# Performance work log

Measured on AMD Instinct MI355X. Metric: run time of the kernel, lower is better.

The kernel has to match this reference:

```python
import jax, jax.numpy as jnp
import numpy as np

N_U, N_D = 64, 64
N_E = N_U + N_D
N_A = 32
N_SV, N_PV = 512, 64
# n1 = [4*N_A, N_SV, N_SV, N_SV]; n2 = [4, N_PV, N_PV, N_PV]


def setup_inputs() -> dict:
    key = jax.random.key(0)
    ks = jax.random.split(key, 32)
    n1 = [4 * N_A, N_SV, N_SV, N_SV]
    n2 = [4, N_PV, N_PV, N_PV]
    d = {}
    d['r'] = jax.random.normal(ks[0], (N_E, 3), jnp.float32)
    d['a'] = jax.random.normal(ks[1], (N_A, 3), jnp.float32)
    i = 2
    for l in range(3):
        fin = 3 * n1[l] + 2 * n2[l]
        d[f'V{l}_w'] = jax.random.normal(ks[i], (fin, n1[l + 1]), jnp.float32) / np.float32(np.sqrt(fin)); i += 1
        d[f'V{l}_b'] = jax.random.normal(ks[i], (n1[l + 1],), jnp.float32); i += 1
        d[f'W{l}_w'] = jax.random.normal(ks[i], (n2[l], n2[l + 1]), jnp.float32) / np.float32(np.sqrt(n2[l])); i += 1
        d[f'W{l}_b'] = jax.random.normal(ks[i], (n2[l + 1],), jnp.float32); i += 1
    fin = 3 * N_SV + 2 * N_PV
    d['after_w'] = jax.random.normal(ks[i], (fin, N_SV), jnp.float32) / np.float32(np.sqrt(fin)); i += 1
    d['after_b'] = jax.random.normal(ks[i], (N_SV,), jnp.float32); i += 1
    d['vhu_w'] = jax.random.normal(ks[i], (N_SV, N_SV // 2), jnp.float32) / np.float32(np.sqrt(N_SV)); i += 1
    d['vhu_b'] = jax.random.normal(ks[i], (N_SV // 2,), jnp.float32); i += 1
    d['vhd_w'] = jax.random.normal(ks[i], (N_SV, N_SV // 2), jnp.float32) / np.float32(np.sqrt(N_SV)); i += 1
    d['vhd_b'] = jax.random.normal(ks[i], (N_SV // 2,), jnp.float32); i += 1
    d['wu_w'] = jax.random.normal(ks[i], (N_SV // 2, N_U), jnp.float32) / np.float32(np.sqrt(N_SV // 2)); i += 1
    d['wu_b'] = jax.random.normal(ks[i], (N_U,), jnp.float32); i += 1
    d['wd_w'] = jax.random.normal(ks[i], (N_SV // 2, N_D), jnp.float32) / np.float32(np.sqrt(N_SV // 2)); i += 1
    d['wd_b'] = jax.random.normal(ks[i], (N_D,), jnp.float32); i += 1
    return d


def _fb_block(s_v, p_v):
    # s_v: (N_E, f_s), p_v: (N_E, N_E, f_p)
    s_u_mean = jnp.tile(s_v[:N_U].mean(0)[None, :], (N_E, 1))
    s_d_mean = jnp.tile(s_v[N_U:].mean(0)[None, :], (N_E, 1))
    p_u_mean = p_v[:N_U].mean(0)  # (N_E, f_p)
    p_d_mean = p_v[N_U:].mean(0)
    return jnp.concatenate([s_u_mean, s_d_mean, p_u_mean, p_d_mean, s_v], axis=-1)


def _forward(r, a, Vw, Vb, Ww, Wb, after_w, after_b, vhu_w, vhu_b, vhd_w, vhd_b, wu_w, wu_b, wd_w, wd_b):
    eye = jnp.eye(N_E, dtype=r.dtype)[:, :, None]
    ra = r[:, None, :] - a[None, :, :]                       # (N_E, N_A, 3)
    ra_len = jnp.linalg.norm(ra, axis=-1, keepdims=True)     # (N_E, N_A, 1)
    rr = r[None, :, :] - r[:, None, :]                       # (N_E, N_E, 3)
    rr_len = jnp.linalg.norm(rr + eye, axis=-1, keepdims=True) * (1.0 - eye)
    s_v = jnp.concatenate([ra, ra_len], axis=-1).reshape(N_E, -1)  # (N_E, 4*N_A)
    p_v = jnp.concatenate([rr, rr_len], axis=-1)                   # (N_E, N_E, 4)
    for vw, vb, ww, wb in zip(Vw, Vb, Ww, Wb):
        s_in = _fb_block(s_v, p_v)
        # NOTE: torch residual `s_v if s_v.shape[-1]==n_sv` never fires here:
        # fb_block output width is 3*n1+2*n2 != n_sv, so it adds zeros.
        s_v = jnp.tanh(s_in @ vw + vb)
        p_new = jnp.tanh(p_v @ ww + wb)
        p_v = p_new + (p_v if p_v.shape[-1] == N_PV else 0.0)
    s_in = _fb_block(s_v, p_v)
    s_v = jnp.tanh(s_in @ after_w + after_b)  # (N_E, N_SV); residual again never fires
    s_u = s_v[:N_U] @ vhu_w + vhu_b
    s_d = s_v[N_U:] @ vhd_w + vhd_b
    s_wu = s_u @ wu_w + wu_b   # (N_U, N_U)
    s_wd = s_d @ wd_w + wd_b   # (N_D, N_D)
    exp_u = jnp.linalg.norm(ra[:N_U], axis=-1, keepdims=True)  # (N_U, N_A, 1)
    exp_d = jnp.linalg.norm(ra[N_U:], axis=-1, keepdims=True)
    orb_u = (s_wu * jnp.exp(-exp_u).sum(axis=1))[None]  # (1, N_U, N_U)
    orb_d = (s_wd * jnp.exp(-exp_d).sum(axis=1))[None]
    # logabssumdet for two (1,n,n) matrices with n>1: no 1x1 dets.
    sgn_u, ld_u = jnp.linalg.slogdet(orb_u)
    sgn_d, ld_d = jnp.linalg.slogdet(orb_d)
    sign = sgn_u * sgn_d
    logdet = ld_u + ld_d        # (1,)
    maxlogdet = logdet.max()
    psi = (sign * jnp.exp(logdet - maxlogdet)).sum()
    return jnp.log(jnp.abs(psi)) + maxlogdet  # scalar log|psi|


def reference(r, a, V0_w, V0_b, V1_w, V1_b, V2_w, V2_b, W0_w, W0_b, W1_w, W1_b, W2_w, W2_b,
              after_w, after_b, vhu_w, vhu_b, vhd_w, vhd_b, wu_w, wu_b, wd_w, wd_b):
    Vw, Vb = [V0_w, V1_w, V2_w], [V0_b, V1_b, V2_b]
    Ww, Wb = [W0_w, W1_w, W2_w], [W0_b, W1_b, W2_b]
    return _forward(r, a, Vw, Vb, Ww, Wb, after_w, after_b,
                    vhu_w, vhu_b, vhd_w, vhd_b, wu_w, wu_b, wd_w, wd_b)
```

## Files before the change

### kernel.cpp

```cpp
#include <hip/hip_runtime.h>
#include <math.h>

#define NSV 512

__device__ void pchain_role(int b, const float* __restrict__ r,
                            const float* __restrict__ apos,
                            const float* __restrict__ W0w, const float* __restrict__ W0b,
                            const float* __restrict__ W1w, const float* __restrict__ W1b,
                            const float* __restrict__ W2w, const float* __restrict__ W2b,
                            float* __restrict__ expv,
                            float* __restrict__ pme1, float* __restrict__ pme2,
                            float* __restrict__ pme3, float* sh)
{
    float* rL    = sh;
    float* W0l   = sh + 384;
    float* aposL = sh + 640;
    float* shex  = sh + 736;
    float* p0c   = sh + 768;
    float* PA    = sh + 1024;
    float* Wbuf  = sh + 5376;
    const int j  = b >> 1, sp = b & 1;
    const int t  = threadIdx.x;
    const int i  = t >> 3;
    const int o0 = (t & 7) * 8;

    if (t < 384) rL[t] = r[t];
    else if (t < 480) aposL[t - 384] = apos[t - 384];
    for (int idx = t; idx < 4096; idx += 512) Wbuf[idx] = W1w[idx];
    if (t < 256) W0l[t] = W0w[t];
    __syncthreads();

    const float rjx = rL[j*3+0], rjy = rL[j*3+1], rjz = rL[j*3+2];
    if (t < 64) {
        const int ii = sp*64 + t;
        float dx = rjx - rL[ii*3+0], dy = rjy - rL[ii*3+1], dz = rjz - rL[ii*3+2];
        float len = (ii == j) ? 0.f : sqrtf(dx*dx + dy*dy + dz*dz);
        p0c[t*4+0]=dx; p0c[t*4+1]=dy; p0c[t*4+2]=dz; p0c[t*4+3]=len;
    } else if (sp == 0 && t < 96) {
        const int k = t - 64;
        float dx = rjx - aposL[k*3+0], dy = rjy - aposL[k*3+1], dz = rjz - aposL[k*3+2];
        shex[k] = expf(-sqrtf(dx*dx + dy*dy + dz*dz));
    }
    __syncthreads();

    {
        const float x0=p0c[i*4+0], x1=p0c[i*4+1], x2=p0c[i*4+2], x3=p0c[i*4+3];
        #pragma unroll
        for (int k = 0; k < 8; ++k) {
            const int o = o0 + k;
            float a = W0b[o];
            a = fmaf(x0, W0l[o],     a);
            a = fmaf(x1, W0l[64+o],  a);
            a = fmaf(x2, W0l[128+o], a);
            a = fmaf(x3, W0l[192+o], a);
            PA[i*68+o] = tanhf(a);
        }
    }
    if (sp == 0 && t == 4) {
        float s = 0.f;
        #pragma unroll 8
        for (int k = 0; k < 32; ++k) s += shex[k];
        expv[j] = s;
    }
    __syncthreads();

    if (t < 64) {
        float s = 0.f;
        #pragma unroll 8
        for (int k = 0; k < 64; ++k) s += PA[k*68 + t];
        pme1[j*128 + sp*64 + t] = s * 0.015625f;
    }
    float acc[8], res[8];
    const float* pa = PA + i*68;
    {
        #pragma unroll
        for (int k = 0; k < 8; ++k) acc[k] = W1b[o0+k];
        #pragma unroll 4
        for (int c = 0; c < 64; ++c) {
            const float av = pa[c];
            const float* wr = Wbuf + c*64 + o0;
            float4 wa = *reinterpret_cast<const float4*>(wr);
            float4 wb = *reinterpret_cast<const float4*>(wr+4);
            acc[0]=fmaf(av,wa.x,acc[0]); acc[1]=fmaf(av,wa.y,acc[1]);
            acc[2]=fmaf(av,wa.z,acc[2]); acc[3]=fmaf(av,wa.w,acc[3]);
            acc[4]=fmaf(av,wb.x,acc[4]); acc[5]=fmaf(av,wb.y,acc[5]);
            acc[6]=fmaf(av,wb.z,acc[6]); acc[7]=fmaf(av,wb.w,acc[7]);
        }
        #pragma unroll
        for (int k = 0; k < 8; ++k) res[k] = pa[o0+k];
    }
    __syncthreads();
    #pragma unroll
    for (int k = 0; k < 8; ++k) PA[i*68+o0+k] = tanhf(acc[k]) + res[k];
    __syncthreads();

    if (t < 64) {
        float s = 0.f;
        #pragma unroll 8
        for (int k = 0; k < 64; ++k) s += PA[k*68 + t];
        pme2[j*128 + sp*64 + t] = s * 0.015625f;
    }
    for (int idx = t; idx < 4096; idx += 512) Wbuf[idx] = W2w[idx];
    __syncthreads();

    {
        #pragma unroll
        for (int k = 0; k < 8; ++k) acc[k] = W2b[o0+k];
        #pragma unroll 4
        for (int c = 0; c < 64; ++c) {
            const float av = pa[c];
            const float* wr = Wbuf + c*64 + o0;
            float4 wa = *reinterpret_cast<const float4*>(wr);
            float4 wb = *reinterpret_cast<const float4*>(wr+4);
            acc[0]=fmaf(av,wa.x,acc[0]); acc[1]=fmaf(av,wa.y,acc[1]);
            acc[2]=fmaf(av,wa.z,acc[2]); acc[3]=fmaf(av,wa.w,acc[3]);
            acc[4]=fmaf(av,wb.x,acc[4]); acc[5]=fmaf(av,wb.y,acc[5]);
            acc[6]=fmaf(av,wb.z,acc[6]); acc[7]=fmaf(av,wb.w,acc[7]);
        }
        #pragma unroll
        for (int k = 0; k < 8; ++k) res[k] = pa[o0+k];
    }
    __syncthreads();
    #pragma unroll
    for (int k = 0; k < 8; ++k) PA[i*68+o0+k] = tanhf(acc[k]) + res[k];
    __syncthreads();

    if (t < 64) {
        float s = 0.f;
        #pragma unroll 8
        for (int k = 0; k < 64; ++k) s += PA[k*68 + t];
        pme3[j*128 + sp*64 + t] = s * 0.015625f;
    }
}

__device__ void a0_role(int ab, const float* __restrict__ r,
                        const float* __restrict__ apos,
                        const float* __restrict__ V0w, const float* __restrict__ V0b,
                        float* __restrict__ svA, float* __restrict__ psA, float* sh)
{
    constexpr int KP = 136, KP2 = 68;
    float* As    = sh;
    float* smL   = sh + 544;
    float* red   = sh + 800;
    float* t1L   = sh + 1312;
    float* rL    = sh + 1376;
    float* aposL = sh + 1760;
    const int t  = threadIdx.x;
    const int et = ab >> 3, e0 = et * 4;
    const int o0 = (ab & 7) * 64;
    const int ol = t & 63, o = o0 + ol;
    const int wv = t >> 6;

    if (t < 384) rL[t] = r[t];
    else if (t < 480) aposL[t - 384] = apos[t - 384];
    __syncthreads();

    if (t < 128) {
        const int e_l = t >> 5, k = t & 31;
        const int e = e0 + e_l;
        float dx = rL[e*3+0]-aposL[k*3+0], dy = rL[e*3+1]-aposL[k*3+1],
              dz = rL[e*3+2]-aposL[k*3+2];
        float len = sqrtf(dx*dx + dy*dy + dz*dz);
        float* dst = As + e_l*KP + 8 + k*4;
        dst[0]=dx; dst[1]=dy; dst[2]=dz; dst[3]=len;
    } else if (t < 160) {
        const int q = t - 128;
        const int e_l = q >> 3, outp = q & 7;
        const int spin = outp >> 2, c = outp & 3;
        const int e = e0 + e_l;
        const float ex = rL[e*3+0], ey = rL[e*3+1], ez = rL[e*3+2];
        float s = 0.f;
        for (int i2 = 0; i2 < 64; ++i2) {
            const int ii = spin*64 + i2;
            float dx = ex - rL[ii*3+0], dy = ey - rL[ii*3+1], dz = ez - rL[ii*3+2];
            float v = (c==0)?dx:(c==1)?dy:(c==2)?dz:
                      ((ii==e)?0.f:sqrtf(dx*dx+dy*dy+dz*dz));
            s += v;
        }
        As[e_l*KP + outp] = s * 0.015625f;
    }
    {
        const int outp = t >> 1, half = t & 1;
        const int spin = outp >> 7, cc = outp & 127, a_i = cc >> 2, d = cc & 3;
        const float ax = aposL[a_i*3+0], ay = aposL[a_i*3+1], az = aposL[a_i*3+2];
        float s = 0.f;
        #pragma unroll 8
        for (int q = 0; q < 32; ++q) {
            const int e = spin*64 + half*32 + q;
            float dx = rL[e*3+0]-ax, dy = rL[e*3+1]-ay, dz = rL[e*3+2]-az;
            float len = sqrtf(dx*dx + dy*dy + dz*dz);
            s += (d==0)?dx:(d==1)?dy:(d==2)?dz:len;
        }
        red[t] = s;
    }
    __syncthreads();
    if (t < 256) smL[t] = (red[2*t] + red[2*t+1]) * 0.015625f;
    __syncthreads();

    {
        float a1 = 0.f;
        const float* Wp = V0w + (size_t)(wv*32)*NSV + o;
        const float* mp = smL + wv*32;
        #pragma unroll 8
        for (int k = 0; k < 32; ++k) a1 = fmaf(mp[k], Wp[(size_t)k*NSV], a1);
        red[wv*64 + ol] = a1;
    }
    __syncthreads();
    if (t < 64) {
        float s = V0b[o0 + t];
        #pragma unroll
        for (int g = 0; g < 8; ++g) s += red[g*64 + t];
        t1L[t] = s;
    }
    __syncthreads();

    const int e_l = wv & 3, kh = wv >> 2;
    {
        float a2 = (kh == 0) ? t1L[ol] : 0.f;
        const float* Ap = As + e_l*KP + kh*KP2;
        const float* Wp = V0w + (size_t)(256 + kh*KP2)*NSV + o;
        #pragma unroll 16
        for (int k = 0; k < KP2; ++k)
            a2 = fmaf(Ap[k], Wp[(size_t)k*NSV], a2);
        red[wv*64 + ol] = a2;
    }
    __syncthreads();
    float v = 0.f;
    if (t < 256) {
        v = tanhf(red[(t>>6)*64 + (t&63)] + red[((t>>6)+4)*64 + (t&63)]);
        svA[(size_t)(e0 + (t>>6))*NSV + o0 + (t&63)] = v;
    }
    __syncthreads();
    if (t < 256) red[t] = v;
    __syncthreads();
    if (t < 64) {
        float s = red[t] + red[64+t] + red[128+t] + red[192+t];
        psA[(size_t)et*NSV + o0 + t] = s;
    }
}

__global__ __launch_bounds__(512)
void front_kernel(const float* __restrict__ r, const float* __restrict__ apos,
                  const float* __restrict__ V0w, const float* __restrict__ V0b,
                  const float* __restrict__ W0w, const float* __restrict__ W0b,
                  const float* __restrict__ W1w, const float* __restrict__ W1b,
                  const float* __restrict__ W2w, const float* __restrict__ W2b,
                  float* __restrict__ svA, float* __restrict__ expv,
                  float* __restrict__ pme1, float* __restrict__ pme2,
                  float* __restrict__ pme3, float* __restrict__ psA)
{
    __shared__ __align__(16) float sh[9472];
    const int b = blockIdx.x;
    if (b < 256)
        pchain_role(b, r, apos, W0w, W0b, W1w, W1b, W2w, W2b,
                    expv, pme1, pme2, pme3, sh);
    else
        a0_role(b - 256, r, apos, V0w, V0b, svA, psA, sh);
}

template<int FS, int FP>
__global__ __launch_bounds__(512)
void a2_kernel(const float* __restrict__ svIn, const float* __restrict__ pmeIn,
               const float* __restrict__ psumIn,
               const float* __restrict__ Vw, const float* __restrict__ Vb,
               float* __restrict__ svOut, float* __restrict__ psumOut)
{
    constexpr int KP  = 2*FP + FS;
    constexpr int KP2 = KP/2;
    __shared__ __align__(16) float As[4*KP];
    __shared__ __align__(16) float smL[2*FS];
    __shared__ __align__(16) float red[512];
    __shared__ float t1L[64];
    const int t  = threadIdx.x;
    const int et = blockIdx.x >> 3;
    const int e0 = et * 4;
    const int o0 = (blockIdx.x & 7) * 64;
    const int ol = t & 63;
    const int o  = o0 + ol;
    const int wv = t >> 6;

    for (int idx = t; idx < 4*2*FP; idx += 512)
        As[(idx/(2*FP))*KP + idx%(2*FP)] =
            pmeIn[(size_t)(e0 + idx/(2*FP))*(2*FP) + idx%(2*FP)];
    for (int idx = t; idx < FS; idx += 512) {
        const int row = idx / (FS/4), c4 = idx % (FS/4);
        *reinterpret_cast<float4*>(&As[row*KP + 2*FP + c4*4]) =
            *reinterpret_cast<const float4*>(&svIn[(size_t)(e0+row)*FS + c4*4]);
    }
    for (int idx = t; idx < 2*FS; idx += 512) {
        const int col = (idx < FS) ? idx : idx - FS;
        const int r0  = (idx < FS) ? 0 : 16;
        const float* base = psumIn + (size_t)r0*NSV + col;
        float s = 0.f;
        #pragma unroll
        for (int k = 0; k < 16; ++k) s += base[(size_t)k*NSV];
        smL[idx] = s * 0.015625f;
    }
    __syncthreads();

    {
        constexpr int TI = (2*FS)/8;
        float a1 = 0.f;
        const float* Wp = Vw + (size_t)(wv*TI)*NSV + o;
        const float* mp = smL + wv*TI;
        #pragma unroll 8
        for (int k = 0; k < TI; ++k) a1 = fmaf(mp[k], Wp[(size_t)k*NSV], a1);
        red[wv*64 + ol] = a1;
    }
    __syncthreads();
    if (t < 64) {
        float s = Vb[o0 + t];
        #pragma unroll
        for (int g = 0; g < 8; ++g) s += red[g*64 + t];
        t1L[t] = s;
    }
    __syncthreads();

    const int e_l = wv & 3, kh = wv >> 2;
    {
        float a2 = (kh == 0) ? t1L[ol] : 0.f;
        const float* Ap = As + e_l*KP + kh*KP2;
        const float* Wp = Vw + (size_t)(2*FS + kh*KP2)*NSV + o;
        #pragma unroll 16
        for (int k = 0; k < KP2; ++k)
            a2 = fmaf(Ap[k], Wp[(size_t)k*NSV], a2);
        red[wv*64 + ol] = a2;
    }
    __syncthreads();
    float v = 0.f;
    if (t < 256) {
        v = tanhf(red[(t>>6)*64 + (t&63)] + red[((t>>6)+4)*64 + (t&63)]);
        svOut[(size_t)(e0 + (t>>6))*NSV + o0 + (t&63)] = v;
    }
    if (psumOut) {
        __syncthreads();
        if (t < 256) red[t] = v;
        __syncthreads();
        if (t < 64) {
            float s = red[t] + red[64+t] + red[128+t] + red[192+t];
            psumOut[(size_t)et*NSV + o0 + t] = s;
        }
    }
}

__global__ __launch_bounds__(512)
void headsw_kernel(const float* __restrict__ svF,
                   const float* __restrict__ vhu_w, const float* __restrict__ vhu_b,
                   const float* __restrict__ vhd_w, const float* __restrict__ vhd_b,
                   const float* __restrict__ wu_w,  const float* __restrict__ wu_b,
                   const float* __restrict__ wd_w,  const float* __restrict__ wd_b,
                   const float* __restrict__ expv,  float* __restrict__ orb)
{
    __shared__ __align__(16) float row[512];
    __shared__ __align__(16) float redH[512];
    __shared__ __align__(16) float tmpL[256];
    const int e = blockIdx.x;
    const int spin = e >> 6;
    const int t = threadIdx.x;
    row[t] = svF[(size_t)e*NSV + t];
    __syncthreads();

    const float* W1 = spin ? vhd_w : vhu_w;
    const float* B1 = spin ? vhd_b : vhu_b;
    {
        const int o = t & 255, kc = t >> 8;
        float acc = kc ? 0.f : B1[o];
        const float* Wp = W1 + (size_t)(kc*256)*256 + o;
        const float* rp = row + kc*256;
        #pragma unroll 8
        for (int f = 0; f < 256; ++f)
            acc = fmaf(rp[f], Wp[(size_t)f*256], acc);
        redH[t] = acc;
    }
    __syncthreads();
    if (t < 256) tmpL[t] = redH[t] + redH[256 + t];
    __syncthreads();

    const float* W2 = spin ? wd_w : wu_w;
    const float* B2 = spin ? wd_b : wu_b;
    {
        const int o = t & 63, kc = t >> 6;
        float acc = 0.f;
        const float* Wp = W2 + (size_t)(kc*32)*64 + o;
        const float* tp = tmpL + kc*32;
        #pragma unroll
        for (int f = 0; f < 32; ++f)
            acc = fmaf(tp[f], Wp[(size_t)f*64], acc);
        redH[kc*64 + o] = acc;
    }
    __syncthreads();
    if (t < 64) {
        float s = B2[t];
        #pragma unroll
        for (int g = 0; g < 8; ++g) s += redH[g*64 + t];
        orb[(size_t)e*64 + t] = s * expv[e];
    }
}

__device__ __forceinline__ int imax2(int a, int b) { return a > b ? a : b; }
__device__ __forceinline__ float readlane_f(float x, int lane) {
    return __int_as_float(__builtin_amdgcn_readlane(__float_as_int(x), lane));
}

__global__ __launch_bounds__(128)
void det_kernel(const float* __restrict__ orb, float* __restrict__ out)
{
    __shared__ float parts[2];
    const int t = threadIdx.x;
    const int w = t >> 6;
    const int lane = t & 63;
    const float* M = orb + (size_t)w*4096 + (size_t)lane*64;
    float rr[64];
    #pragma unroll
    for (int j = 0; j < 64; j += 4) {
        float4 v = *reinterpret_cast<const float4*>(M + j);
        rr[j]=v.x; rr[j+1]=v.y; rr[j+2]=v.z; rr[j+3]=v.w;
    }
    float pv_mine = 1.f;
    bool active = true;
    #pragma unroll
    for (int k = 0; k < 64; ++k) {
        int bits = (int)(__float_as_uint(rr[k]) & 0x7FFFFFC0u);
        int v = active ? (bits | lane) : lane;
        int tmp;
        tmp = __builtin_amdgcn_update_dpp(0, v, 0xB1,  0xF, 0xF, true); v = imax2(v, tmp);
        tmp = __builtin_amdgcn_update_dpp(0, v, 0x4E,  0xF, 0xF, true); v = imax2(v, tmp);
        tmp = __builtin_amdgcn_update_dpp(0, v, 0x141, 0xF, 0xF, true); v = imax2(v, tmp);
        tmp = __builtin_amdgcn_update_dpp(0, v, 0x140, 0xF, 0xF, true); v = imax2(v, tmp);
        tmp = __builtin_amdgcn_update_dpp(0, v, 0x142, 0xF, 0xF, true); v = imax2(v, tmp);
        tmp = __builtin_amdgcn_update_dpp(0, v, 0x143, 0xF, 0xF, true); v = imax2(v, tmp);
        const int idx = __builtin_amdgcn_readlane(v, 63) & 63;
        const float piv = readlane_f(rr[k], idx);
        pv_mine = (lane == k) ? piv : pv_mine;
        const float linv = __builtin_amdgcn_rcpf(piv);
        const float l = (active && lane != idx) ? rr[k]*linv : 0.f;
        if (lane == idx) active = false;
        #pragma unroll
        for (int j = k+1; j < 64; ++j)
            rr[j] = fmaf(-l, readlane_f(rr[j], idx), rr[j]);
    }
    float lg = logf(fabsf(pv_mine));
    #pragma unroll
    for (int off = 32; off; off >>= 1) lg += __shfl_down(lg, off);
    if (lane == 0) parts[w] = lg;
    __syncthreads();
    if (t == 0) out[0] = parts[0] + parts[1];
}

extern "C" void kernel_launch(void* const* d_in, const int* in_sizes, int n_in,
                              void* d_out, int out_size, void* d_ws, size_t ws_size,
                              hipStream_t stream)
{
    const float* r    = (const float*)d_in[0];
    const float* apos = (const float*)d_in[1];
    const float* V0w  = (const float*)d_in[2];
    const float* V0b  = (const float*)d_in[3];
    const float* W0w  = (const float*)d_in[4];
    const float* W0b  = (const float*)d_in[5];
    const float* V1w  = (const float*)d_in[6];
    const float* V1b  = (const float*)d_in[7];
    const float* W1w  = (const float*)d_in[8];
    const float* W1b  = (const float*)d_in[9];
    const float* V2w  = (const float*)d_in[10];
    const float* V2b  = (const float*)d_in[11];
    const float* W2w  = (const float*)d_in[12];
    const float* W2b  = (const float*)d_in[13];
    const float* afw  = (const float*)d_in[14];
    const float* afb  = (const float*)d_in[15];
    const float* vhuw = (const float*)d_in[16];
    const float* vhub = (const float*)d_in[17];
    const float* vhdw = (const float*)d_in[18];
    const float* vhdb = (const float*)d_in[19];
    const float* wuw  = (const float*)d_in[20];
    const float* wub  = (const float*)d_in[21];
    const float* wdw  = (const float*)d_in[22];
    const float* wdb  = (const float*)d_in[23];

    float* ws   = (float*)d_ws;
    float* svA  = ws;
    float* svB  = svA  + 65536;
    float* expv = svB  + 65536;
    float* pme1 = expv + 128;
    float* pme2 = pme1 + 16384;
    float* pme3 = pme2 + 16384;
    float* psA  = pme3 + 16384;
    float* psB  = psA  + 16384;
    float* orb  = psB  + 16384;

    front_kernel<<<512, 512, 0, stream>>>(r, apos, V0w, V0b, W0w, W0b,
                                          W1w, W1b, W2w, W2b,
                                          svA, expv, pme1, pme2, pme3, psA);
    a2_kernel<512, 64><<<256, 512, 0, stream>>>(svA, pme1, psA, V1w, V1b, svB, psB);
    a2_kernel<512, 64><<<256, 512, 0, stream>>>(svB, pme2, psB, V2w, V2b, svA, psA);
    a2_kernel<512, 64><<<256, 512, 0, stream>>>(svA, pme3, psA, afw, afb, svB, nullptr);
    headsw_kernel<<<128, 512, 0, stream>>>(svB, vhuw, vhub, vhdw, vhdb,
                                           wuw, wub, wdw, wdb, expv, orb);
    det_kernel<<<1, 128, 0, stream>>>(orb, (float*)d_out);
}
```

Baseline: 101.7 us.

## Precompose linear head weights and fuse head projection into final layer kernel

```diff
diff --git a/kernel.cpp b/kernel.cpp
--- a/kernel.cpp
+++ b/kernel.cpp
@@ -239,23 +239,88 @@
     }
 }
 
+__device__ void headc_role(int g, const float* __restrict__ vh,
+                           const float* __restrict__ wu,
+                           float* __restrict__ Cdst, float* sh)
+{
+    float* wuL = sh;
+    float* vhL = sh + 4096;
+    const int t = threadIdx.x;
+    const int o2 = t & 63, wq = t >> 6;
+    const int f0 = g * 16;
+    float a0 = 0.f, a1 = 0.f;
+    for (int hc = 0; hc < 4; ++hc) {
+        __syncthreads();
+        for (int idx = t; idx < 4096; idx += 512)
+            wuL[idx] = wu[(size_t)(hc*64 + (idx>>6))*64 + (idx&63)];
+        for (int idx = t; idx < 1024; idx += 512)
+            vhL[idx] = vh[(size_t)(f0 + (idx>>6))*256 + hc*64 + (idx&63)];
+        __syncthreads();
+        #pragma unroll 8
+        for (int h = 0; h < 64; ++h) {
+            const float wuv = wuL[h*64 + o2];
+            a0 = fmaf(vhL[wq*64 + h],     wuv, a0);
+            a1 = fmaf(vhL[(wq+8)*64 + h], wuv, a1);
+        }
+    }
+    Cdst[(size_t)(f0 + wq)*64 + o2]     = a0;
+    Cdst[(size_t)(f0 + wq + 8)*64 + o2] = a1;
+}
+
+__device__ void cb_role(const float* __restrict__ vhb, const float* __restrict__ wu,
+                        const float* __restrict__ wub, float* __restrict__ cbdst,
+                        float* sh)
+{
+    const int t = threadIdx.x;
+    const int o2 = t & 63, wq = t >> 6;
+    float acc = 0.f;
+    #pragma unroll
+    for (int k = 0; k < 32; ++k) {
+        const int h = wq*32 + k;
+        acc = fmaf(vhb[h], wu[(size_t)h*64 + o2], acc);
+    }
+    sh[t] = acc;
+    __syncthreads();
+    if (t < 64) {
+        float s = wub[t];
+        #pragma unroll
+        for (int g = 0; g < 8; ++g) s += sh[g*64 + t];
+        cbdst[t] = s;
+    }
+}
+
 __global__ __launch_bounds__(512)
 void front_kernel(const float* __restrict__ r, const float* __restrict__ apos,
                   const float* __restrict__ V0w, const float* __restrict__ V0b,
                   const float* __restrict__ W0w, const float* __restrict__ W0b,
                   const float* __restrict__ W1w, const float* __restrict__ W1b,
                   const float* __restrict__ W2w, const float* __restrict__ W2b,
+                  const float* __restrict__ vhuw, const float* __restrict__ vhub,
+                  const float* __restrict__ vhdw, const float* __restrict__ vhdb,
+                  const float* __restrict__ wuw,  const float* __restrict__ wub,
+                  const float* __restrict__ wdw,  const float* __restrict__ wdb,
                   float* __restrict__ svA, float* __restrict__ expv,
                   float* __restrict__ pme1, float* __restrict__ pme2,
-                  float* __restrict__ pme3, float* __restrict__ psA)
+                  float* __restrict__ pme3, float* __restrict__ psA,
+                  float* __restrict__ Cmat, float* __restrict__ cb)
 {
     __shared__ __align__(16) float sh[9472];
     const int b = blockIdx.x;
-    if (b < 256)
+    if (b < 256) {
         pchain_role(b, r, apos, W0w, W0b, W1w, W1b, W2w, W2b,
                     expv, pme1, pme2, pme3, sh);
-    else
+    } else if (b < 512) {
         a0_role(b - 256, r, apos, V0w, V0b, svA, psA, sh);
+    } else if (b < 576) {
+        const int g = b - 512;
+        const int spin = g >> 5;
+        headc_role(g & 31, spin ? vhdw : vhuw, spin ? wdw : wuw,
+                   Cmat + (size_t)spin*32768, sh);
+    } else {
+        const int spin = b - 576;
+        cb_role(spin ? vhdb : vhub, spin ? wdw : wuw, spin ? wdb : wub,
+                cb + spin*64, sh);
+    }
 }
 
 template<int FS, int FP>
@@ -263,8 +328,99 @@
 void a2_kernel(const float* __restrict__ svIn, const float* __restrict__ pmeIn,
                const float* __restrict__ psumIn,
                const float* __restrict__ Vw, const float* __restrict__ Vb,
-               float* __restrict__ svOut, float* __restrict__ psumOut)
-{
+               float* __restrict__ svOut, float* __restrict__ psumOut,
+               float* __restrict__ orbInit, const float* __restrict__ cb)
+{
+    constexpr int KP  = 2*FP + FS;
+    constexpr int KP2 = KP/2;
+    __shared__ __align__(16) float As[4*KP];
+    __shared__ __align__(16) float smL[2*FS];
+    __shared__ __align__(16) float red[512];
+    __shared__ float t1L[64];
+    const int t  = threadIdx.x;
+    if (blockIdx.x >= 256) {
+        for (int idx = t; idx < 8192; idx += 512)
+            orbInit[idx] = cb[(((idx >> 6) >> 6) << 6) + (idx & 63)];
+        return;
+    }
+    const int et = blockIdx.x >> 3;
+    const int e0 = et * 4;
+    const int o0 = (blockIdx.x & 7) * 64;
+    const int ol = t & 63;
+    const int o  = o0 + ol;
+    const int wv = t >> 6;
+
+    for (int idx = t; idx < 4*2*FP; idx += 512)
+        As[(idx/(2*FP))*KP + idx%(2*FP)] =
+            pmeIn[(size_t)(e0 + idx/(2*FP))*(2*FP) + idx%(2*FP)];
+    for (int idx = t; idx < FS; idx += 512) {
+        const int row = idx / (FS/4), c4 = idx % (FS/4);
+        *reinterpret_cast<float4*>(&As[row*KP + 2*FP + c4*4]) =
+            *reinterpret_cast<const float4*>(&svIn[(size_t)(e0+row)*FS + c4*4]);
+    }
+    for (int idx = t; idx < 2*FS; idx += 512) {
+        const int col = (idx < FS) ? idx : idx - FS;
+        const int r0  = (idx < FS) ? 0 : 16;
+        const float* base = psumIn + (size_t)r0*NSV + col;
+        float s = 0.f;
+        #pragma unroll
+        for (int k = 0; k < 16; ++k) s += base[(size_t)k*NSV];
+        smL[idx] = s * 0.015625f;
+    }
+    __syncthreads();
+
+    {
+        constexpr int TI = (2*FS)/8;
+        float a1 = 0.f;
+        const float* Wp = Vw + (size_t)(wv*TI)*NSV + o;
+        const float* mp = smL + wv*TI;
+        #pragma unroll 8
+        for (int k = 0; k < TI; ++k) a1 = fmaf(mp[k], Wp[(size_t)k*NSV], a1);
+        red[wv*64 + ol] = a1;
+    }
+    __syncthreads();
+    if (t < 64) {
+        float s = Vb[o0 + t];
+        #pragma unroll
+        for (int g = 0; g < 8; ++g) s += red[g*64 + t];
+        t1L[t] = s;
+    }
+    __syncthreads();
+
+    const int e_l = wv & 3, kh = wv >> 2;
+    {
+        float a2 = (kh == 0) ? t1L[ol] : 0.f;
+        const float* Ap = As + e_l*KP + kh*KP2;
+        const float* Wp = Vw + (size_t)(2*FS + kh*KP2)*NSV + o;
+        #pragma unroll 16
+        for (int k = 0; k < KP2; ++k)
+            a2 = fmaf(Ap[k], Wp[(size_t)k*NSV], a2);
+        red[wv*64 + ol] = a2;
+    }
+    __syncthreads();
+    float v = 0.f;
+    if (t < 256) {
+        v = tanhf(red[(t>>6)*64 + (t&63)] + red[((t>>6)+4)*64 + (t&63)]);
+        svOut[(size_t)(e0 + (t>>6))*NSV + o0 + (t&63)] = v;
+    }
+    if (psumOut) {
+        __syncthreads();
+        if (t < 256) red[t] = v;
+        __syncthreads();
+        if (t < 64) {
+            float s = red[t] + red[64+t] + red[128+t] + red[192+t];
+            psumOut[(size_t)et*NSV + o0 + t] = s;
+        }
+    }
+}
+
+__global__ __launch_bounds__(512)
+void a3h_kernel(const float* __restrict__ svIn, const float* __restrict__ pmeIn,
+                const float* __restrict__ psumIn,
+                const float* __restrict__ Vw, const float* __restrict__ Vb,
+                const float* __restrict__ Cmat, float* __restrict__ orb)
+{
+    constexpr int FS = 512, FP = 64;
     constexpr int KP  = 2*FP + FS;
     constexpr int KP2 = KP/2;
     __shared__ __align__(16) float As[4*KP];
@@ -328,72 +484,21 @@
     }
     __syncthreads();
     float v = 0.f;
+    if (t < 256)
+        v = tanhf(red[(t>>6)*64 + (t&63)] + red[((t>>6)+4)*64 + (t&63)]);
+    __syncthreads();
+    if (t < 256) smL[t] = v;
+    __syncthreads();
     if (t < 256) {
-        v = tanhf(red[(t>>6)*64 + (t&63)] + red[((t>>6)+4)*64 + (t&63)]);
-        svOut[(size_t)(e0 + (t>>6))*NSV + o0 + (t&63)] = v;
-    }
-    if (psumOut) {
-        __syncthreads();
-        if (t < 256) red[t] = v;
-        __syncthreads();
-        if (t < 64) {
-            float s = red[t] + red[64+t] + red[128+t] + red[192+t];
-            psumOut[(size_t)et*NSV + o0 + t] = s;
-        }
-    }
-}
-
-__global__ __launch_bounds__(512)
-void headsw_kernel(const float* __restrict__ svF,
-                   const float* __restrict__ vhu_w, const float* __restrict__ vhu_b,
-                   const float* __restrict__ vhd_w, const float* __restrict__ vhd_b,
-                   const float* __restrict__ wu_w,  const float* __restrict__ wu_b,
-                   const float* __restrict__ wd_w,  const float* __restrict__ wd_b,
-                   const float* __restrict__ expv,  float* __restrict__ orb)
-{
-    __shared__ __align__(16) float row[512];
-    __shared__ __align__(16) float redH[512];
-    __shared__ __align__(16) float tmpL[256];
-    const int e = blockIdx.x;
-    const int spin = e >> 6;
-    const int t = threadIdx.x;
-    row[t] = svF[(size_t)e*NSV + t];
-    __syncthreads();
-
-    const float* W1 = spin ? vhd_w : vhu_w;
-    const float* B1 = spin ? vhd_b : vhu_b;
-    {
-        const int o = t & 255, kc = t >> 8;
-        float acc = kc ? 0.f : B1[o];
-        const float* Wp = W1 + (size_t)(kc*256)*256 + o;
-        const float* rp = row + kc*256;
-        #pragma unroll 8
-        for (int f = 0; f < 256; ++f)
-            acc = fmaf(rp[f], Wp[(size_t)f*256], acc);
-        redH[t] = acc;
-    }
-    __syncthreads();
-    if (t < 256) tmpL[t] = redH[t] + redH[256 + t];
-    __syncthreads();
-
-    const float* W2 = spin ? wd_w : wu_w;
-    const float* B2 = spin ? wd_b : wu_b;
-    {
-        const int o = t & 63, kc = t >> 6;
+        const int el2 = t >> 6, o2 = t & 63;
+        const int spin = et >> 4;
+        const float* Cp = Cmat + (size_t)spin*32768 + (size_t)o0*64 + o2;
+        const float* sp = smL + el2*64;
         float acc = 0.f;
-        const float* Wp = W2 + (size_t)(kc*32)*64 + o;
-        const float* tp = tmpL + kc*32;
-        #pragma unroll
-        for (int f = 0; f < 32; ++f)
-            acc = fmaf(tp[f], Wp[(size_t)f*64], acc);
-        redH[kc*64 + o] = acc;
-    }
-    __syncthreads();
-    if (t < 64) {
-        float s = B2[t];
-        #pragma unroll
-        for (int g = 0; g < 8; ++g) s += redH[g*64 + t];
-        orb[(size_t)e*64 + t] = s * expv[e];
+        #pragma unroll 8
+        for (int f = 0; f < 64; ++f)
+            acc = fmaf(sp[f], Cp[(size_t)f*64], acc);
+        atomicAdd(&orb[(size_t)(e0 + el2)*64 + o2], acc);
     }
 }
 
@@ -403,18 +508,20 @@
 }
 
 __global__ __launch_bounds__(128)
-void det_kernel(const float* __restrict__ orb, float* __restrict__ out)
+void det_kernel(const float* __restrict__ orb, const float* __restrict__ expv,
+                float* __restrict__ out)
 {
     __shared__ float parts[2];
     const int t = threadIdx.x;
     const int w = t >> 6;
     const int lane = t & 63;
     const float* M = orb + (size_t)w*4096 + (size_t)lane*64;
+    const float ex = expv[w*64 + lane];
     float rr[64];
     #pragma unroll
     for (int j = 0; j < 64; j += 4) {
         float4 v = *reinterpret_cast<const float4*>(M + j);
-        rr[j]=v.x; rr[j+1]=v.y; rr[j+2]=v.z; rr[j+3]=v.w;
+        rr[j]=v.x*ex; rr[j+1]=v.y*ex; rr[j+2]=v.z*ex; rr[j+3]=v.w*ex;
     }
     float pv_mine = 1.f;
     bool active = true;
@@ -486,14 +593,19 @@
     float* psA  = pme3 + 16384;
     float* psB  = psA  + 16384;
     float* orb  = psB  + 16384;
-
-    front_kernel<<<512, 512, 0, stream>>>(r, apos, V0w, V0b, W0w, W0b,
+    float* Cmat = orb  + 8192;
+    float* cb   = Cmat + 65536;
+
+    front_kernel<<<578, 512, 0, stream>>>(r, apos, V0w, V0b, W0w, W0b,
                                           W1w, W1b, W2w, W2b,
-                                          svA, expv, pme1, pme2, pme3, psA);
-    a2_kernel<512, 64><<<256, 512, 0, stream>>>(svA, pme1, psA, V1w, V1b, svB, psB);
-    a2_kernel<512, 64><<<256, 512, 0, stream>>>(svB, pme2, psB, V2w, V2b, svA, psA);
-    a2_kernel<512, 64><<<256, 512, 0, stream>>>(svA, pme3, psA, afw, afb, svB, nullptr);
-    headsw_kernel<<<128, 512, 0, stream>>>(svB, vhuw, vhub, vhdw, vhdb,
-                                           wuw, wub, wdw, wdb, expv, orb);
-    det_kernel<<<1, 128, 0, stream>>>(orb, (float*)d_out);
-}
+                                          vhuw, vhub, vhdw, vhdb,
+                                          wuw, wub, wdw, wdb,
+                                          svA, expv, pme1, pme2, pme3, psA,
+                                          Cmat, cb);
+    a2_kernel<512, 64><<<257, 512, 0, stream>>>(svA, pme1, psA, V1w, V1b,
+                                                svB, psB, orb, cb);
+    a2_kernel<512, 64><<<256, 512, 0, stream>>>(svB, pme2, psB, V2w, V2b,
+                                                svA, psA, nullptr, nullptr);
+    a3h_kernel<<<256, 512, 0, stream>>>(svA, pme3, psA, afw, afb, Cmat, orb);
+    det_kernel<<<1, 128, 0, stream>>>(orb, expv, (float*)d_out);
+}
```

Result: faster. 91.68 us (-9.9%).
